# Kernel tuning notes

Hardware: AMD Instinct MI355X
Metric: run time of the kernel (lower is better)

## Reference

```python
import jax, jax.numpy as jnp
import numpy as np

B, C, F, D = 128, 16, 128, 512


def setup_inputs() -> dict:
    key = jax.random.key(0)
    k1, k2 = jax.random.split(key)
    return {
        "c_feats": jax.random.normal(k1, (B, C, D), dtype=jnp.float32),
        "f_feats": jax.random.normal(k2, (B, F, D), dtype=jnp.float32),
    }


def _dtw_path_masks(S):
    """S: [P, c, f] per-pair similarity. Returns [P, c, f] 0/1 max-path masks.

    DP: D[i,j] = max(D[i-1,j], D[i,j-1], D[i-1,j-1]) + S[i-1,j-1], D[0,0]=0,
    borders -inf. Tie-break priority (up, left, diag) matches Python max().
    Row recurrence is vectorized: D[i,j] = Csum[j] + cummax_k<=j(A[k]-Csum[k-1])
    where A[k]=max(D[i-1,k], D[i-1,k-1]) (wavefront-free row-parallel form).
    """
    P_, c, f = S.shape
    NEG = -jnp.inf

    init = jnp.concatenate([jnp.zeros((P_, 1), S.dtype),
                            jnp.full((P_, f), NEG, S.dtype)], axis=1)  # D[0, 0..f]

    def row_step(prev, dt_row):
        # prev: [P, f+1] = D[i-1, 0..f]; dt_row: [P, f] = S[i-1, :]
        A = jnp.maximum(prev[:, 1:], prev[:, :-1])                  # max(D[i-1,j], D[i-1,j-1])
        Ccum = jnp.cumsum(dt_row, axis=1)
        Cm1 = jnp.concatenate([jnp.zeros((P_, 1), dt_row.dtype), Ccum[:, :-1]], axis=1)
        row = Ccum + jax.lax.cummax(A - Cm1, axis=1)                # D[i, 1..f]
        new_prev = jnp.concatenate([jnp.full((P_, 1), NEG, dt_row.dtype), row], axis=1)
        return new_prev, new_prev

    _, rows = jax.lax.scan(row_step, init, jnp.moveaxis(S, 1, 0))   # [c, P, f+1]
    Dm = jnp.moveaxis(jnp.concatenate([init[None], rows], axis=0), 1, 0)  # [P, c+1, f+1]

    # Predecessor choice per cell; argmax picks first max -> priority up,left,diag
    up = Dm[:, :-1, 1:]
    left = Dm[:, 1:, :-1]
    diag = Dm[:, :-1, :-1]
    mv = jnp.argmax(jnp.stack([up, left, diag], axis=-1), axis=-1).astype(jnp.int32)
    mv = jnp.pad(mv, ((0, 0), (1, 0), (1, 0)))                      # [P, c+1, f+1]

    pidx = jnp.arange(P_)

    def bt_step(carry, _):
        mask, i, j = carry
        active = (i > 0) | (j > 0)
        mask = mask.at[pidx, i - 1, j - 1].add(jnp.where(active, 1.0, 0.0).astype(mask.dtype))
        m = mv[pidx, i, j]
        di = jnp.where(m == 1, 0, 1)   # left keeps i
        dj = jnp.where(m == 0, 0, 1)   # up keeps j
        i = jnp.where(active, i - di, i)
        j = jnp.where(active, j - dj, j)
        return (mask, i, j), None

    mask0 = jnp.zeros((P_, c, f), jnp.float32)
    i0 = jnp.full((P_,), c, jnp.int32)
    j0 = jnp.full((P_,), f, jnp.int32)
    (mask, _, _), _ = jax.lax.scan(bt_step, (mask0, i0, j0), None, length=c + f)
    return mask


def reference(c_feats, f_feats):
    b, c, d = c_feats.shape
    f = f_feats.shape[1]
    xn = c_feats / jnp.linalg.norm(c_feats, axis=-1, keepdims=True)
    yn = f_feats / jnp.linalg.norm(f_feats, axis=-1, keepdims=True)
    # Source quirk: y row j is normalized only once outer index i reaches it
    # (y[i-1] bug), so S[i,j] uses normalized y[j] iff j <= i, raw y[j] otherwise.
    Sn = jnp.einsum('mcd,nfd->mncf', xn, yn)
    Sr = jnp.einsum('mcd,nfd->mncf', xn, f_feats)
    tri = jnp.arange(f)[None, :] <= jnp.arange(c)[:, None]          # [c, f]: j <= i
    S = jnp.where(tri, Sn, Sr).reshape(b * b, c, f)
    return _dtw_path_masks(S).reshape(b, b, c, f)
```

## Files before the change

kernel.cpp:

```cpp
#include <hip/hip_runtime.h>
#include <stdint.h>

#define M_TOT 2048
#define N_TOT 16384
#define K_TOT 512

typedef _Float16 f16x8 __attribute__((ext_vector_type(8)));
typedef float f32x16 __attribute__((ext_vector_type(16)));

#define AS1 __attribute__((address_space(1)))
#define AS3 __attribute__((address_space(3)))

__device__ __forceinline__ void ld_lds16(const void* g, void* l) {
    __builtin_amdgcn_global_load_lds((const AS1 void*)g, (AS3 void*)l, 16, 0, 0);
}

__device__ __forceinline__ void split4(float x0, float x1, float x2, float x3,
                                       uint2* hs, uint2* ls) {
    union U { _Float16 h[4]; uint2 u; } H, L;
    _Float16 h0 = (_Float16)x0; H.h[0] = h0; L.h[0] = (_Float16)(x0 - (float)h0);
    _Float16 h1 = (_Float16)x1; H.h[1] = h1; L.h[1] = (_Float16)(x1 - (float)h1);
    _Float16 h2 = (_Float16)x2; H.h[2] = h2; L.h[2] = (_Float16)(x2 - (float)h2);
    _Float16 h3 = (_Float16)x3; H.h[3] = h3; L.h[3] = (_Float16)(x3 - (float)h3);
    *hs = H.u; *ls = L.u;
}

__global__ __launch_bounds__(256) void norm_split_kernel(
    const float* __restrict__ c_feats, const float* __restrict__ f_feats,
    _Float16* __restrict__ Ah, _Float16* __restrict__ Al,
    _Float16* __restrict__ Bh, _Float16* __restrict__ Bl,
    float* __restrict__ normf)
{
    int wave = blockIdx.x * 4 + (threadIdx.x >> 6);
    int lane = threadIdx.x & 63;
    if (wave < 2048) {
        const float* row = c_feats + (size_t)wave * K_TOT;
        float4 v0 = ((const float4*)row)[lane];
        float4 v1 = ((const float4*)row)[lane + 64];
        double ss = (double)v0.x * v0.x + (double)v0.y * v0.y +
                    (double)v0.z * v0.z + (double)v0.w * v0.w +
                    (double)v1.x * v1.x + (double)v1.y * v1.y +
                    (double)v1.z * v1.z + (double)v1.w * v1.w;
        #pragma unroll
        for (int off = 32; off; off >>= 1) ss += __shfl_down(ss, off);
        double tot = __shfl(ss, 0);
        float nrm = sqrtf((float)tot);
        float a0 = v0.x / nrm, a1 = v0.y / nrm, a2 = v0.z / nrm, a3 = v0.w / nrm;
        float b0 = v1.x / nrm, b1 = v1.y / nrm, b2 = v1.z / nrm, b3 = v1.w / nrm;
        uint2 h, l;
        split4(a0, a1, a2, a3, &h, &l);
        ((uint2*)(Ah + (size_t)wave * K_TOT))[lane] = h;
        ((uint2*)(Al + (size_t)wave * K_TOT))[lane] = l;
        split4(b0, b1, b2, b3, &h, &l);
        ((uint2*)(Ah + (size_t)wave * K_TOT))[lane + 64] = h;
        ((uint2*)(Al + (size_t)wave * K_TOT))[lane + 64] = l;
    } else if (wave < 18432) {
        int fr = wave - 2048;
        const float* row = f_feats + (size_t)fr * K_TOT;
        float4 v0 = ((const float4*)row)[lane];
        float4 v1 = ((const float4*)row)[lane + 64];
        double ss = (double)v0.x * v0.x + (double)v0.y * v0.y +
                    (double)v0.z * v0.z + (double)v0.w * v0.w +
                    (double)v1.x * v1.x + (double)v1.y * v1.y +
                    (double)v1.z * v1.z + (double)v1.w * v1.w;
        #pragma unroll
        for (int off = 32; off; off >>= 1) ss += __shfl_down(ss, off);
        if (lane == 0) normf[fr] = sqrtf((float)ss);
        uint2 h, l;
        split4(v0.x, v0.y, v0.z, v0.w, &h, &l);
        ((uint2*)(Bh + (size_t)fr * K_TOT))[lane] = h;
        ((uint2*)(Bl + (size_t)fr * K_TOT))[lane] = l;
        split4(v1.x, v1.y, v1.z, v1.w, &h, &l);
        ((uint2*)(Bh + (size_t)fr * K_TOT))[lane + 64] = h;
        ((uint2*)(Bl + (size_t)fr * K_TOT))[lane + 64] = l;
    }
}

__global__ __launch_bounds__(256, 4) void mfma_gemm_kernel(
    const _Float16* __restrict__ Ah, const _Float16* __restrict__ Al,
    const _Float16* __restrict__ Bh, const _Float16* __restrict__ Bl,
    const float* __restrict__ normf,
    float* __restrict__ out)
{
    __shared__ _Float16 sAh[128 * 32];
    __shared__ _Float16 sAl[128 * 32];
    __shared__ _Float16 sBh[128 * 32];
    __shared__ _Float16 sBl[128 * 32];

    const int t = threadIdx.x;
    const int w = t >> 6, lane = t & 63;
    const int ntile = ((blockIdx.x & 7) << 4) | (blockIdx.x >> 3);
    const int gm0 = blockIdx.y * 128, gn0 = ntile * 128;
    const int wm = (w & 1) * 64, wn = (w >> 1) * 64;
    const int m32 = lane & 31;
    const int kql0 = lane >> 5;

    f32x16 acc[2][2] = {};
    const int l0 = w * 128 + lane;

    for (int k0 = 0; k0 < K_TOT; k0 += 32) {
        #pragma unroll
        for (int c = 0; c < 2; ++c) {
            int l = l0 + c * 64;
            int lrow = l >> 2, kq = l & 3;
            int kqs = kq ^ ((lrow >> 1) & 3);
            size_t goffA = (size_t)(gm0 + lrow) * K_TOT + k0 + kqs * 8;
            size_t goffB = (size_t)(gn0 + lrow) * K_TOT + k0 + kqs * 8;
            ld_lds16(Ah + goffA, sAh + (size_t)l * 8);
            ld_lds16(Al + goffA, sAl + (size_t)l * 8);
            ld_lds16(Bh + goffB, sBh + (size_t)l * 8);
            ld_lds16(Bl + goffB, sBl + (size_t)l * 8);
        }
        __syncthreads();

        #pragma unroll
        for (int kh = 0; kh < 2; ++kh) {
            f16x8 fah[2], fal[2], fbh[2], fbl[2];
            #pragma unroll
            for (int x = 0; x < 2; ++x) {
                int arr = wm + x * 32 + m32;
                int brr = wn + x * 32 + m32;
                int kqa = (kh * 2 + kql0) ^ ((arr >> 1) & 3);
                int kqb = (kh * 2 + kql0) ^ ((brr >> 1) & 3);
                int ar = arr * 32 + kqa * 8;
                int br = brr * 32 + kqb * 8;
                fah[x] = *(const f16x8*)(sAh + ar);
                fal[x] = *(const f16x8*)(sAl + ar);
                fbh[x] = *(const f16x8*)(sBh + br);
                fbl[x] = *(const f16x8*)(sBl + br);
            }
            #pragma unroll
            for (int mi = 0; mi < 2; ++mi)
                #pragma unroll
                for (int ni = 0; ni < 2; ++ni) {
                    acc[mi][ni] = __builtin_amdgcn_mfma_f32_32x32x16_f16(fah[mi], fbl[ni], acc[mi][ni], 0, 0, 0);
                    acc[mi][ni] = __builtin_amdgcn_mfma_f32_32x32x16_f16(fal[mi], fbh[ni], acc[mi][ni], 0, 0, 0);
                    acc[mi][ni] = __builtin_amdgcn_mfma_f32_32x32x16_f16(fah[mi], fbh[ni], acc[mi][ni], 0, 0, 0);
                }
        }
        __syncthreads();
    }

    const int nn = ntile;
    const int rq = 4 * (lane >> 5);
    #pragma unroll
    for (int ni = 0; ni < 2; ++ni) {
        int col = wn + ni * 32 + m32;
        bool cn = (col < 16);
        float nf = cn ? normf[gn0 + col] : 1.f;
        #pragma unroll
        for (int mi = 0; mi < 2; ++mi) {
            #pragma unroll
            for (int reg = 0; reg < 16; ++reg) {
                int r = wm + mi * 32 + (reg & 3) + 8 * (reg >> 2) + rq;
                int gm = gm0 + r;
                int mm = gm >> 4, ii = gm & 15;
                float v = acc[mi][ni][reg];
                if (cn && col <= ii) v /= nf;
                out[(((size_t)mm * 128 + nn) * 16 + ii) * 128 + col] = v;
            }
        }
    }
}

#define WQS 304
#define WBUF 1216

__device__ __forceinline__ float dpp_shr1_f32(float x) {
    union { float f; int i; } u, v;
    u.f = x;
    v.i = __builtin_amdgcn_update_dpp(u.i, u.i, 0x111, 0xF, 0xF, false);
    return v.f;
}

__global__ __launch_bounds__(64) void dtw_kernel(float* __restrict__ buf)
{
    __shared__ float swin[2 * WBUF];
    __shared__ uint32_t mvw[4][132];
    __shared__ int bounds[4][16];

    const int lane = threadIdx.x & 63;
    const int q = lane >> 4, r = lane & 15;
    const int pbase = (4095 - (int)blockIdx.x) * 4;
    const float4* gbase = (const float4*)(buf + (size_t)pbase * 2048);
    float* sw = swin;
    uint32_t* mvq = &mvw[q][0];

    int gidx[4], lidx[4];
    #pragma unroll
    for (int i = 0; i < 4; ++i) {
        gidx[i] = i * 512 + ((lane >> 2) & 15) * 32 + (lane & 3);
        lidx[i] = i * WQS + ((lane >> 2) & 15) * 18 + (lane & 3) * 4;
    }

#define WSTORE(regs, boff)                                                      \
    {                                                                           \
        _Pragma("unroll")                                                       \
        for (int i = 0; i < 4; ++i) {                                           \
            *(float2*)(sw + (boff) + lidx[i])     = make_float2(regs[i].x, regs[i].y); \
            *(float2*)(sw + (boff) + lidx[i] + 2) = make_float2(regs[i].z, regs[i].w); \
        }                                                                       \
    }
#define WLOAD(regs, win)                                                        \
    {                                                                           \
        _Pragma("unroll")                                                       \
        for (int i = 0; i < 4; ++i) regs[i] = gbase[gidx[i] + (win) * 4];       \
    }

    float4 ga[4], gb[4];
    WLOAD(ga, 0)
    WLOAD(gb, 1)
    WSTORE(ga, 0)
    WSTORE(gb, WBUF)
    WLOAD(ga, 2)
    WLOAD(gb, 3)

    const float NEG = -1e30f;
    float Dp = NEG, rawprev = NEG;
    uint32_t mvbuf = 0;
    int j = -r;
    const int sb = q * WQS + r * 18;

#define DTW_STEP(BOUNDARY)                                                      \
    {                                                                           \
        float upr = dpp_shr1_f32(Dp);                                           \
        float dg = rawprev;                                                     \
        rawprev = upr;                                                          \
        float up = (r == 0) ? NEG : upr;                                        \
        float lf = Dp;                                                          \
        if (BOUNDARY) {                                                         \
            if (j == 0) { lf = NEG; dg = (r == 0) ? 0.0f : NEG; }               \
            else if (r == 0) dg = NEG;                                          \
        } else {                                                                \
            if (r == 0) dg = NEG;                                               \
        }                                                                       \
        float sv = sw[(((j >> 4) & 1) ? WBUF : 0) + sb + (j & 15)];             \
        int m = (up >= lf && up >= dg) ? 0 : ((lf >= dg) ? 1 : 2);              \
        float Dc = fmaxf(up, fmaxf(lf, dg)) + sv;                               \
        if ((unsigned)j < 128u) {                                               \
            mvbuf |= (uint32_t)m << (2 * (j & 15));                             \
            if ((j & 15) == 15) { mvq[r * 8 + (j >> 4)] = mvbuf; mvbuf = 0; }   \
        }                                                                       \
        Dp = Dc;                                                                \
        ++j;                                                                    \
    }

    for (int t = 0; t < 16; ++t) DTW_STEP(true)
    for (int t = 16; t < 32; ++t) DTW_STEP(false)
    WSTORE(ga, 0)        WLOAD(ga, 4)
    for (int t = 32; t < 48; ++t) DTW_STEP(false)
    WSTORE(gb, WBUF)     WLOAD(gb, 5)
    for (int t = 48; t < 64; ++t) DTW_STEP(false)
    WSTORE(ga, 0)        WLOAD(ga, 6)
    for (int t = 64; t < 80; ++t) DTW_STEP(false)
    WSTORE(gb, WBUF)     WLOAD(gb, 7)
    for (int t = 80; t < 96; ++t) DTW_STEP(false)
    WSTORE(ga, 0)
    for (int t = 96; t < 112; ++t) DTW_STEP(false)
    WSTORE(gb, WBUF)
    for (int t = 112; t < 143; ++t) DTW_STEP(false)
#undef DTW_STEP
#undef WSTORE
#undef WLOAD

    __syncthreads();

    if (r == 0) {
        int i = 16, jj = 128, hic = 127;
        int cidx = -1;
        uint32_t word = 0;
        for (int it = 0; it < 160; ++it) {
            if (i <= 0) break;
            int idx = (i - 1) * 8 + ((jj - 1) >> 4);
            if (idx != cidx) { word = mvq[idx]; cidx = idx; }
            int m = (int)((word >> (2 * ((jj - 1) & 15))) & 3u);
            if (m == 1) { --jj; continue; }
            bounds[q][i - 1] = (jj - 1) | (hic << 8);
            if (m == 2) --jj;
            --i;
            hic = jj - 1;
        }
    }
    __syncthreads();

    #pragma unroll 4
    for (int it = 0; it < 32; ++it) {
        int flat = it * 64 + lane;
        int q2 = flat >> 9;
        int rem = flat & 511;
        int ii = rem >> 5;
        int c4 = rem & 31;
        int b = bounds[q2][ii];
        int lo = b & 0xff, hi = (b >> 8) & 0xff;
        int j0 = c4 * 4;
        float4 v;
        v.x = (j0 + 0 >= lo && j0 + 0 <= hi) ? 1.f : 0.f;
        v.y = (j0 + 1 >= lo && j0 + 1 <= hi) ? 1.f : 0.f;
        v.z = (j0 + 2 >= lo && j0 + 2 <= hi) ? 1.f : 0.f;
        v.w = (j0 + 3 >= lo && j0 + 3 <= hi) ? 1.f : 0.f;
        float* tb = buf + (size_t)(pbase + q2) * 2048;
        *(float4*)(tb + ii * 128 + j0) = v;
    }
}

extern "C" void kernel_launch(void* const* d_in, const int* in_sizes, int n_in,
                              void* d_out, int out_size, void* d_ws, size_t ws_size,
                              hipStream_t stream)
{
    const float* c_feats = (const float*)d_in[0];
    const float* f_feats = (const float*)d_in[1];
    float* out = (float*)d_out;

    _Float16* Ah = (_Float16*)d_ws;
    _Float16* Al = Ah + (size_t)M_TOT * K_TOT;
    _Float16* Bh = Al + (size_t)M_TOT * K_TOT;
    _Float16* Bl = Bh + (size_t)N_TOT * K_TOT;
    float* normf = (float*)(Bl + (size_t)N_TOT * K_TOT);

    norm_split_kernel<<<4608, 256, 0, stream>>>(c_feats, f_feats, Ah, Al, Bh, Bl, normf);
    dim3 g(N_TOT / 128, M_TOT / 128);
    mfma_gemm_kernel<<<g, 256, 0, stream>>>(Ah, Al, Bh, Bl, normf, out);
    dtw_kernel<<<4096, 64, 0, stream>>>(out);
}
```

Measured before the change: 336.6 us.

## Rewrite split-fp16 GEMM with 256x256 tiles and double-buffered LDS pipeline

```diff
diff --git a/kernel.cpp b/kernel.cpp
--- a/kernel.cpp
+++ b/kernel.cpp
@@ -14,6 +14,10 @@
 __device__ __forceinline__ void ld_lds16(const void* g, void* l) {
     __builtin_amdgcn_global_load_lds((const AS1 void*)g, (AS3 void*)l, 16, 0, 0);
 }
+
+#define BAR() do { asm volatile("" ::: "memory"); __builtin_amdgcn_s_barrier(); asm volatile("" ::: "memory"); } while (0)
+#define VMC4() asm volatile("s_waitcnt vmcnt(4)" ::: "memory")
+#define VMC0() asm volatile("s_waitcnt vmcnt(0)" ::: "memory")
 
 __device__ __forceinline__ void split4(float x0, float x1, float x2, float x3,
                                        uint2* hs, uint2* ls) {
@@ -76,85 +80,163 @@
     }
 }
 
-__global__ __launch_bounds__(256, 4) void mfma_gemm_kernel(
+__global__ __launch_bounds__(512, 2) void mfma_gemm_kernel(
     const _Float16* __restrict__ Ah, const _Float16* __restrict__ Al,
     const _Float16* __restrict__ Bh, const _Float16* __restrict__ Bl,
     const float* __restrict__ normf,
     float* __restrict__ out)
 {
-    __shared__ _Float16 sAh[128 * 32];
-    __shared__ _Float16 sAl[128 * 32];
-    __shared__ _Float16 sBh[128 * 32];
-    __shared__ _Float16 sBl[128 * 32];
+    __shared__ _Float16 lds[2 * 4 * 8192];
 
     const int t = threadIdx.x;
     const int w = t >> 6, lane = t & 63;
-    const int ntile = ((blockIdx.x & 7) << 4) | (blockIdx.x >> 3);
-    const int gm0 = blockIdx.y * 128, gn0 = ntile * 128;
-    const int wm = (w & 1) * 64, wn = (w >> 1) * 64;
-    const int m32 = lane & 31;
-    const int kql0 = lane >> 5;
-
-    f32x16 acc[2][2] = {};
-    const int l0 = w * 128 + lane;
-
-    for (int k0 = 0; k0 < K_TOT; k0 += 32) {
-        #pragma unroll
-        for (int c = 0; c < 2; ++c) {
-            int l = l0 + c * 64;
-            int lrow = l >> 2, kq = l & 3;
-            int kqs = kq ^ ((lrow >> 1) & 3);
-            size_t goffA = (size_t)(gm0 + lrow) * K_TOT + k0 + kqs * 8;
-            size_t goffB = (size_t)(gn0 + lrow) * K_TOT + k0 + kqs * 8;
-            ld_lds16(Ah + goffA, sAh + (size_t)l * 8);
-            ld_lds16(Al + goffA, sAl + (size_t)l * 8);
-            ld_lds16(Bh + goffB, sBh + (size_t)l * 8);
-            ld_lds16(Bl + goffB, sBl + (size_t)l * 8);
-        }
-        __syncthreads();
-
-        #pragma unroll
-        for (int kh = 0; kh < 2; ++kh) {
-            f16x8 fah[2], fal[2], fbh[2], fbl[2];
-            #pragma unroll
-            for (int x = 0; x < 2; ++x) {
-                int arr = wm + x * 32 + m32;
-                int brr = wn + x * 32 + m32;
-                int kqa = (kh * 2 + kql0) ^ ((arr >> 1) & 3);
-                int kqb = (kh * 2 + kql0) ^ ((brr >> 1) & 3);
-                int ar = arr * 32 + kqa * 8;
-                int br = brr * 32 + kqb * 8;
-                fah[x] = *(const f16x8*)(sAh + ar);
-                fal[x] = *(const f16x8*)(sAl + ar);
-                fbh[x] = *(const f16x8*)(sBh + br);
-                fbl[x] = *(const f16x8*)(sBl + br);
-            }
-            #pragma unroll
-            for (int mi = 0; mi < 2; ++mi)
-                #pragma unroll
-                for (int ni = 0; ni < 2; ++ni) {
-                    acc[mi][ni] = __builtin_amdgcn_mfma_f32_32x32x16_f16(fah[mi], fbl[ni], acc[mi][ni], 0, 0, 0);
-                    acc[mi][ni] = __builtin_amdgcn_mfma_f32_32x32x16_f16(fal[mi], fbh[ni], acc[mi][ni], 0, 0, 0);
-                    acc[mi][ni] = __builtin_amdgcn_mfma_f32_32x32x16_f16(fah[mi], fbh[ni], acc[mi][ni], 0, 0, 0);
-                }
-        }
-        __syncthreads();
-    }
-
-    const int nn = ntile;
-    const int rq = 4 * (lane >> 5);
+    const int m32 = lane & 31, kql0 = lane >> 5;
+    const int wr = w >> 2, wc = w & 3;
+    const int wm = wr * 128, wn = wc * 64;
+
+    const int bx = (int)blockIdx.x;
+    const int ntile = ((bx & 7) << 3) | (bx >> 3);
+    const int gm0 = (int)blockIdx.y * 256, gn0 = ntile * 256;
+
+    const int rowA = t >> 2;
+    const int kq8 = ((t & 3) ^ ((rowA >> 1) & 3)) * 8;
+    const _Float16* const gA  = Ah + (size_t)(gm0 + rowA) * K_TOT + kq8;
+    const _Float16* const gB  = Bh + (size_t)(gn0 + rowA) * K_TOT + kq8;
+    const _Float16* const gAl2 = gA + (size_t)M_TOT * K_TOT;
+    const _Float16* const gBl2 = gB + (size_t)N_TOT * K_TOT;
+    const int t8 = t * 8;
+
+    int aof[4][2], bof[2][2];
+    #pragma unroll
+    for (int mi = 0; mi < 4; ++mi) {
+        int rr = wm + mi * 32 + m32;
+        int x = (rr >> 1) & 3;
+        #pragma unroll
+        for (int kc = 0; kc < 2; ++kc)
+            aof[mi][kc] = rr * 32 + (((kc * 2 + kql0) ^ x) * 8);
+    }
     #pragma unroll
     for (int ni = 0; ni < 2; ++ni) {
-        int col = wn + ni * 32 + m32;
-        bool cn = (col < 16);
-        float nf = cn ? normf[gn0 + col] : 1.f;
-        #pragma unroll
-        for (int mi = 0; mi < 2; ++mi) {
+        int rr = wn + ni * 32 + m32;
+        int x = (rr >> 1) & 3;
+        #pragma unroll
+        for (int kc = 0; kc < 2; ++kc)
+            bof[ni][kc] = rr * 32 + (((kc * 2 + kql0) ^ x) * 8);
+    }
+
+    f32x16 acc[4][2] = {};
+
+    {
+        _Float16* L0 = lds + t8;
+        ld_lds16(gA,            L0);
+        ld_lds16(gA  + 65536,   L0 + 4096);
+        ld_lds16(gBl2,          L0 + 3 * 8192);
+        ld_lds16(gBl2 + 65536,  L0 + 3 * 8192 + 4096);
+        ld_lds16(gAl2,          L0 + 1 * 8192);
+        ld_lds16(gAl2 + 65536,  L0 + 1 * 8192 + 4096);
+        ld_lds16(gB,            L0 + 2 * 8192);
+        ld_lds16(gB  + 65536,   L0 + 2 * 8192 + 4096);
+        VMC4();
+        BAR();
+    }
+
+    #pragma unroll 1
+    for (int tt = 0; tt < 16; ++tt) {
+        const int cb = (tt & 1) << 15;
+        const _Float16* Lc = lds + cb;
+        _Float16* Ln = lds + (cb ^ 32768) + t8;
+        const int kk = tt * 32 + 32;
+        const bool st = (tt < 15);
+
+        f16x8 faH[4][2], fbH[2][2], faL[4][2], fbL[2][2];
+
+        #pragma unroll
+        for (int mi = 0; mi < 4; ++mi)
+            #pragma unroll
+            for (int kc = 0; kc < 2; ++kc)
+                faH[mi][kc] = *(const f16x8*)(Lc + aof[mi][kc]);
+        #pragma unroll
+        for (int ni = 0; ni < 2; ++ni)
+            #pragma unroll
+            for (int kc = 0; kc < 2; ++kc)
+                fbL[ni][kc] = *(const f16x8*)(Lc + 3 * 8192 + bof[ni][kc]);
+        if (st) {
+            ld_lds16(gA   + kk,         Ln);
+            ld_lds16(gA   + kk + 65536, Ln + 4096);
+            ld_lds16(gBl2 + kk,         Ln + 3 * 8192);
+            ld_lds16(gBl2 + kk + 65536, Ln + 3 * 8192 + 4096);
+        }
+        BAR();
+        __builtin_amdgcn_s_setprio(1);
+        #pragma unroll
+        for (int mi = 0; mi < 4; ++mi)
+            #pragma unroll
+            for (int ni = 0; ni < 2; ++ni)
+                #pragma unroll
+                for (int kc = 0; kc < 2; ++kc)
+                    acc[mi][ni] = __builtin_amdgcn_mfma_f32_32x32x16_f16(
+                        faH[mi][kc], fbL[ni][kc], acc[mi][ni], 0, 0, 0);
+        __builtin_amdgcn_s_setprio(0);
+        if (st) VMC4(); else VMC0();
+        BAR();
+
+        #pragma unroll
+        for (int mi = 0; mi < 4; ++mi)
+            #pragma unroll
+            for (int kc = 0; kc < 2; ++kc)
+                faL[mi][kc] = *(const f16x8*)(Lc + 1 * 8192 + aof[mi][kc]);
+        #pragma unroll
+        for (int ni = 0; ni < 2; ++ni)
+            #pragma unroll
+            for (int kc = 0; kc < 2; ++kc)
+                fbH[ni][kc] = *(const f16x8*)(Lc + 2 * 8192 + bof[ni][kc]);
+        if (st) {
+            ld_lds16(gAl2 + kk,         Ln + 1 * 8192);
+            ld_lds16(gAl2 + kk + 65536, Ln + 1 * 8192 + 4096);
+            ld_lds16(gB   + kk,         Ln + 2 * 8192);
+            ld_lds16(gB   + kk + 65536, Ln + 2 * 8192 + 4096);
+        }
+        BAR();
+        __builtin_amdgcn_s_setprio(1);
+        #pragma unroll
+        for (int mi = 0; mi < 4; ++mi)
+            #pragma unroll
+            for (int ni = 0; ni < 2; ++ni)
+                #pragma unroll
+                for (int kc = 0; kc < 2; ++kc)
+                    acc[mi][ni] = __builtin_amdgcn_mfma_f32_32x32x16_f16(
+                        faL[mi][kc], fbH[ni][kc], acc[mi][ni], 0, 0, 0);
+        __builtin_amdgcn_s_setprio(0);
+        BAR();
+
+        __builtin_amdgcn_s_setprio(1);
+        #pragma unroll
+        for (int mi = 0; mi < 4; ++mi)
+            #pragma unroll
+            for (int ni = 0; ni < 2; ++ni)
+                #pragma unroll
+                for (int kc = 0; kc < 2; ++kc)
+                    acc[mi][ni] = __builtin_amdgcn_mfma_f32_32x32x16_f16(
+                        faH[mi][kc], fbH[ni][kc], acc[mi][ni], 0, 0, 0);
+        __builtin_amdgcn_s_setprio(0);
+        if (st) VMC4();
+        BAR();
+    }
+
+    const int rq = 4 * kql0;
+    #pragma unroll
+    for (int ni = 0; ni < 2; ++ni) {
+        const int gc = gn0 + wn + ni * 32 + m32;
+        const int nn = gc >> 7;
+        const int col = gc & 127;
+        const bool cn = (col < 16);
+        const float nf = cn ? normf[gc] : 1.f;
+        #pragma unroll
+        for (int mi = 0; mi < 4; ++mi) {
             #pragma unroll
             for (int reg = 0; reg < 16; ++reg) {
-                int r = wm + mi * 32 + (reg & 3) + 8 * (reg >> 2) + rq;
-                int gm = gm0 + r;
-                int mm = gm >> 4, ii = gm & 15;
+                const int gm = gm0 + wm + mi * 32 + (reg & 3) + 8 * (reg >> 2) + rq;
+                const int mm = gm >> 4, ii = gm & 15;
                 float v = acc[mi][ni][reg];
                 if (cn && col <= ii) v /= nf;
                 out[(((size_t)mm * 128 + nn) * 16 + ii) * 128 + col] = v;
@@ -245,20 +327,20 @@
         ++j;                                                                    \
     }
 
-    for (int t = 0; t < 16; ++t) DTW_STEP(true)
-    for (int t = 16; t < 32; ++t) DTW_STEP(false)
-    WSTORE(ga, 0)        WLOAD(ga, 4)
-    for (int t = 32; t < 48; ++t) DTW_STEP(false)
-    WSTORE(gb, WBUF)     WLOAD(gb, 5)
-    for (int t = 48; t < 64; ++t) DTW_STEP(false)
-    WSTORE(ga, 0)        WLOAD(ga, 6)
-    for (int t = 64; t < 80; ++t) DTW_STEP(false)
-    WSTORE(gb, WBUF)     WLOAD(gb, 7)
-    for (int t = 80; t < 96; ++t) DTW_STEP(false)
+    for (int tt = 0; tt < 16; ++tt) DTW_STEP(true)
+    for (int tt = 16; tt < 32; ++tt) DTW_STEP(false)
+    WSTORE(ga, 0)      WLOAD(ga, 4)
+    for (int tt = 32; tt < 48; ++tt) DTW_STEP(false)
+    WSTORE(gb, WBUF)   WLOAD(gb, 5)
+    for (int tt = 48; tt < 64; ++tt) DTW_STEP(false)
+    WSTORE(ga, 0)      WLOAD(ga, 6)
+    for (int tt = 64; tt < 80; ++tt) DTW_STEP(false)
+    WSTORE(gb, WBUF)   WLOAD(gb, 7)
+    for (int tt = 80; tt < 96; ++tt) DTW_STEP(false)
     WSTORE(ga, 0)
-    for (int t = 96; t < 112; ++t) DTW_STEP(false)
+    for (int tt = 96; tt < 112; ++tt) DTW_STEP(false)
     WSTORE(gb, WBUF)
-    for (int t = 112; t < 143; ++t) DTW_STEP(false)
+    for (int tt = 112; tt < 143; ++tt) DTW_STEP(false)
 #undef DTW_STEP
 #undef WSTORE
 #undef WLOAD
@@ -318,7 +400,7 @@
     float* normf = (float*)(Bl + (size_t)N_TOT * K_TOT);
 
     norm_split_kernel<<<4608, 256, 0, stream>>>(c_feats, f_feats, Ah, Al, Bh, Bl, normf);
-    dim3 g(N_TOT / 128, M_TOT / 128);
-    mfma_gemm_kernel<<<g, 256, 0, stream>>>(Ah, Al, Bh, Bl, normf, out);
+    dim3 g(N_TOT / 256, M_TOT / 256);
+    mfma_gemm_kernel<<<g, 512, 0, stream>>>(Ah, Al, Bh, Bl, normf, out);
     dtw_kernel<<<4096, 64, 0, stream>>>(out);
 }
```

Result: no change. 333.4 us (-1.0%).
